# Optimization experiments

Measured on AMD Instinct MI355X. Metric: run time of the kernel, lower is better.

## Reference

```python
import jax, jax.numpy as jnp
import numpy as np

EPS = 1e-8

def setup_inputs() -> dict:
    key = jax.random.key(0)
    ks = jax.random.split(key, 7)
    B, S, H, NH, V = 4, 2048, 1024, 8, 2048
    sc = 1.0 / np.sqrt(H)
    return {
        "hidden": jax.random.normal(ks[0], (B, S, H), jnp.float32),
        "prior_w": jax.random.normal(ks[1], (H, NH), jnp.float32) * sc,
        "prior_b": jnp.zeros((NH,), jnp.float32),
        "latent_w": jax.random.normal(ks[2], (H, NH * H), jnp.float32) * sc,
        "latent_b": jnp.zeros((NH * H,), jnp.float32),
        "output_w": jax.random.normal(ks[3], (H, V), jnp.float32) * sc,
        "output_b": jnp.zeros((V,), jnp.float32),
    }

def reference(hidden, prior_w, prior_b, latent_w, latent_b, output_w, output_b):
    B, S, H = hidden.shape
    NH = prior_w.shape[1]
    # prior: sigmoid then renormalize over heads
    prior = jax.nn.sigmoid(hidden @ prior_w + prior_b)              # [B,S,NH]
    prior = prior / (prior.sum(-1, keepdims=True) + EPS)
    # latent: linear -> [B,S,NH,H] -> tanh
    latent = jnp.tanh((hidden @ latent_w + latent_b).reshape(B, S, NH, H))
    # per-head softmax over vocab, weighted sum over heads
    logits = jnp.einsum('bsnh,hv->bsnv', latent, output_w) + output_b
    probs = jax.nn.softmax(logits, axis=-1)                          # [B,S,NH,V]
    return jnp.einsum('bsn,bsnv->bsv', prior, probs)
```

## Files before the change

### kernel.cpp

```cpp
#include <hip/hip_runtime.h>
#include <hip/hip_bf16.h>
#include <stdint.h>

typedef _Float16 f16;
typedef _Float16 f16x8 __attribute__((ext_vector_type(8)));
typedef _Float16 f16x4 __attribute__((ext_vector_type(4)));
typedef float f32x4 __attribute__((ext_vector_type(4)));
typedef float f32x16 __attribute__((ext_vector_type(16)));

#define T_TOK 8192
#define H_DIM 1024
#define NHEAD 8
#define V_DIM 2048

__device__ __forceinline__ void gload16(const void* g, void* l) {
  __builtin_amdgcn_global_load_lds(
      (const __attribute__((address_space(1))) void*)(uintptr_t)g,
      (__attribute__((address_space(3))) void*)(unsigned)(uintptr_t)l,
      16, 0, 0);
}

__device__ __forceinline__ float fast_tanh(float x) {
  float xc = fminf(fmaxf(x, -12.f), 12.f);
  float e = __expf(2.f * xc);
  return (e - 1.f) / (e + 1.f);
}

__device__ __forceinline__ void stage_half(const f16* __restrict__ gRowBase,
                                           char* ldsHalf, int tid, int sl8,
                                           int Kd) {
  const int srow = tid >> 3;
  char* wuni = ldsHalf + ((tid >> 6) << 10);
  gload16(gRowBase + (size_t)srow * Kd + sl8, wuni);
  gload16(gRowBase + (size_t)(srow + 64) * Kd + sl8, wuni + 8192);
}

template <int TANH>
__global__ __launch_bounds__(512, 2) void k_gemm(const f16* __restrict__ A,
                                                 const f16* __restrict__ Bt,
                                                 const float* __restrict__ bias,
                                                 f16* __restrict__ C,
                                                 int M, int N, int K) {
  __shared__ __align__(16) f16 sA[2][16384];
  __shared__ __align__(16) f16 sB[2][16384];
  const int tid = threadIdx.x;
  const int lane = tid & 63;
  const int wid = tid >> 6;
  const int wr = wid >> 2, wc = wid & 3;
  const int id = blockIdx.y * 8 + blockIdx.x;
  const int cpx = gridDim.y;
  const int sw = (id & 7) * cpx + (id >> 3);
  const int m0 = (sw >> 3) * 256;
  const int n0 = blockIdx.z * 2048 + (sw & 7) * 256;
  const int NT = K >> 6;
  const int sl8 = ((tid & 7) ^ ((tid >> 3) & 7)) << 3;
  const int rr31 = lane & 31;
  const int hi = lane >> 5;
  const int l7 = lane & 7;

  const f16* Ag = A + (size_t)m0 * K;
  const f16* Bg = Bt + (size_t)n0 * K;
  char* sAb = (char*)&sA[0][0];
  char* sBb = (char*)&sB[0][0];

  stage_half(Ag, sAb, tid, sl8, K);
  stage_half(Ag + (size_t)128 * K, sAb + 16384, tid, sl8, K);
  stage_half(Bg, sBb, tid, sl8, K);
  stage_half(Bg + (size_t)128 * K, sBb + 16384, tid, sl8, K);
  stage_half(Bg + 64, sBb + 32768, tid, sl8, K);
  stage_half(Bg + (size_t)128 * K + 64, sBb + 32768 + 16384, tid, sl8, K);
  asm volatile("s_waitcnt vmcnt(4)" ::: "memory");
  __builtin_amdgcn_s_barrier();
  __builtin_amdgcn_sched_barrier(0);

  f32x16 acc[4][2] = {};
  f16x8 af0[4], af1[4], bf[2][4];

#define LDA_SET(dst, base, q)                                                  \
  {                                                                            \
    _Pragma("unroll") for (int mi = 0; mi < 4; ++mi) {                         \
      dst[mi] = *(const f16x8*)((base) + wr * 16384 + mi * 4096 + rr31 * 128 + \
                                (((2 * (q) + hi) ^ l7) << 4));                 \
    }                                                                          \
  }
#define LDB(base)                                                              \
  {                                                                            \
    _Pragma("unroll") for (int n = 0; n < 2; ++n) {                            \
      _Pragma("unroll") for (int ks = 0; ks < 4; ++ks) {                       \
        bf[n][ks] = *(const f16x8*)((base) + wc * 8192 + n * 4096 +            \
                                    rr31 * 128 + (((2 * ks + hi) ^ l7) << 4)); \
      }                                                                        \
    }                                                                          \
  }
#define MFMA8(ks, S)                                                           \
  {                                                                            \
    __builtin_amdgcn_s_setprio(1);                                             \
    _Pragma("unroll") for (int mi = 0; mi < 4; ++mi) {                         \
      _Pragma("unroll") for (int n = 0; n < 2; ++n) {                          \
        acc[mi][n] = __builtin_amdgcn_mfma_f32_32x32x16_f16(                   \
            S[mi], bf[n][ks], acc[mi][n], 0, 0, 0);                            \
      }                                                                        \
    }                                                                          \
    __builtin_amdgcn_s_setprio(0);                                             \
  }

  LDA_SET(af0, sAb, 0);

#define HALF(tt, bc)                                                           \
  {                                                                            \
    const char* cA = sAb + (bc)*32768;                                         \
    const char* cB = sBb + (bc)*32768;                                         \
    char* nA = sAb + ((bc) ^ 1) * 32768;                                       \
    char* nB = sBb + (bc)*32768;                                               \
    const int ktA = ((tt) + 1) << 6, ktB = ((tt) + 2) << 6;                    \
    const bool doA = (tt) + 1 < NT, doB = (tt) + 2 < NT;                       \
                                                                      \
    if (doA) stage_half(Ag + ktA, nA, tid, sl8, K);                            \
    LDB(cB);                                                                   \
    LDA_SET(af1, cA, 1);                                                       \
    __builtin_amdgcn_sched_barrier(0);                                         \
    MFMA8(0, af0);                                                             \
    __builtin_amdgcn_s_barrier();                                              \
                                                                      \
    if (doA) stage_half(Ag + (size_t)128 * K + ktA, nA + 16384, tid, sl8, K);  \
    LDA_SET(af0, cA, 2);                                                       \
    __builtin_amdgcn_sched_barrier(0);                                         \
    MFMA8(1, af1);                                                             \
    __builtin_amdgcn_s_barrier();                                              \
                                                                      \
    if (doB) stage_half(Bg + ktB, nB, tid, sl8, K);                            \
    LDA_SET(af1, cA, 3);                                                       \
    __builtin_amdgcn_sched_barrier(0);                                         \
    MFMA8(2, af0);                                                             \
    __builtin_amdgcn_s_barrier();                                              \
                  \
    if (doB) stage_half(Bg + (size_t)128 * K + ktB, nB + 16384, tid, sl8, K);  \
    if (doB) {                                                                 \
      asm volatile("s_waitcnt vmcnt(4)" ::: "memory");                         \
    } else {                                                                   \
      asm volatile("s_waitcnt vmcnt(0)" ::: "memory");                         \
    }                                                                          \
    __builtin_amdgcn_s_barrier();                                              \
    __builtin_amdgcn_sched_barrier(0);                                         \
    if (doA) LDA_SET(af0, sAb + ((bc) ^ 1) * 32768, 0);                        \
    __builtin_amdgcn_sched_barrier(0);                                         \
    MFMA8(3, af1);                                                             \
  }

#pragma unroll 1
  for (int T = 0; T < NT; T += 2) {
    HALF(T, 0);
    HALF(T + 1, 1);
  }
#undef HALF
#undef LDA_SET
#undef LDB
#undef MFMA8

  const int ccol0 = n0 + wc * 64 + rr31;
  float bv[2];
#pragma unroll
  for (int n = 0; n < 2; ++n) bv[n] = bias[ccol0 + n * 32];
#pragma unroll
  for (int mi = 0; mi < 4; ++mi) {
#pragma unroll
    for (int rq = 0; rq < 4; ++rq) {
#pragma unroll
      for (int r2 = 0; r2 < 4; ++r2) {
        const int row = m0 + wr * 128 + mi * 32 + r2 + 8 * rq + 4 * hi;
        f16* Crow = C + (size_t)row * N;
#pragma unroll
        for (int n = 0; n < 2; ++n) {
          float v = acc[mi][n][rq * 4 + r2] + bv[n];
          if (TANH) v = fast_tanh(v);
          Crow[ccol0 + n * 32] = (f16)v;
        }
      }
    }
  }
}

__global__ __launch_bounds__(256) void k_transpose(const float* __restrict__ in,
                                                   f16* __restrict__ out,
                                                   int R, int C) {
  __shared__ f16 tile[64][66];
  const int c0 = blockIdx.x * 64, r0 = blockIdx.y * 64;
  const int tid = threadIdx.x;
  const int tr = tid >> 4;
  const int tc4 = (tid & 15) * 4;
#pragma unroll
  for (int i = 0; i < 4; ++i) {
    const int r = tr + i * 16;
    const float4 v = *(const float4*)&in[(size_t)(r0 + r) * C + c0 + tc4];
    tile[tc4 + 0][r] = (f16)v.x;
    tile[tc4 + 1][r] = (f16)v.y;
    tile[tc4 + 2][r] = (f16)v.z;
    tile[tc4 + 3][r] = (f16)v.w;
  }
  __syncthreads();
  const int oc = tid >> 2;
  const int or4 = (tid & 3) * 16;
#pragma unroll
  for (int i = 0; i < 4; ++i) {
    f16x4 w;
    w[0] = tile[oc][or4 + i * 4 + 0];
    w[1] = tile[oc][or4 + i * 4 + 1];
    w[2] = tile[oc][or4 + i * 4 + 2];
    w[3] = tile[oc][or4 + i * 4 + 3];
    *(f16x4*)&out[(size_t)(c0 + oc) * R + r0 + or4 + i * 4] = w;
  }
}

__global__ __launch_bounds__(256) void k_prior_conv(const float* __restrict__ hidden,
                                                    const float* __restrict__ pw,
                                                    const float* __restrict__ pb,
                                                    float* __restrict__ prior,
                                                    f16* __restrict__ hidden_h) {
  const int wid = threadIdx.x >> 6, lane = threadIdx.x & 63;
  const int t = blockIdx.x * 4 + wid;
  const float* hrow = hidden + (size_t)t * H_DIM;
  f16* orow = hidden_h + (size_t)t * H_DIM;
  float acc[NHEAD] = {0.f, 0.f, 0.f, 0.f, 0.f, 0.f, 0.f, 0.f};
#pragma unroll
  for (int i = 0; i < 4; ++i) {
    const int k = i * 256 + lane * 4;
    const float4 v = *(const float4*)(hrow + k);
    f16x4 o;
    o[0] = (f16)v.x; o[1] = (f16)v.y; o[2] = (f16)v.z; o[3] = (f16)v.w;
    *(f16x4*)(orow + k) = o;
    const float vv[4] = {v.x, v.y, v.z, v.w};
#pragma unroll
    for (int j = 0; j < 4; ++j) {
      const float* wr = pw + (size_t)(k + j) * NHEAD;
#pragma unroll
      for (int h = 0; h < NHEAD; ++h) acc[h] += vv[j] * wr[h];
    }
  }
#pragma unroll
  for (int h = 0; h < NHEAD; ++h) {
#pragma unroll
    for (int off = 32; off >= 1; off >>= 1) acc[h] += __shfl_xor(acc[h], off);
  }
  if (lane == 0) {
    float p[NHEAD], s = 0.f;
#pragma unroll
    for (int h = 0; h < NHEAD; ++h) {
      p[h] = 1.f / (1.f + __expf(-(acc[h] + pb[h])));
      s += p[h];
    }
    float inv = 1.f / (s + 1e-8f);
#pragma unroll
    for (int h = 0; h < NHEAD; ++h) prior[t * NHEAD + h] = p[h] * inv;
  }
}

__global__ __launch_bounds__(256) void k_softmax(const f16* __restrict__ logits,
                                                 const float* __restrict__ prior,
                                                 float* __restrict__ out,
                                                 int t0) {
  __shared__ float redsm[NHEAD * 4];
  const int tl = blockIdx.x;
  const int t = t0 + tl;
  const int tid = threadIdx.x, lane = tid & 63, wid = tid >> 6;
  const f16* base = logits + (size_t)tl * NHEAD * V_DIM + tid * 8;

  f16x8 x[NHEAD];
#pragma unroll
  for (int h = 0; h < NHEAD; ++h) x[h] = *(const f16x8*)(base + h * V_DIM);

  float xv[NHEAD][8];
  float sml[NHEAD];
#pragma unroll
  for (int h = 0; h < NHEAD; ++h) {
    float s = 0.f;
#pragma unroll
    for (int j = 0; j < 8; ++j) {
      xv[h][j] = __expf(fminf((float)x[h][j], 50.f));
      s += xv[h][j];
    }
    sml[h] = s;
  }
#pragma unroll
  for (int h = 0; h < NHEAD; ++h) {
#pragma unroll
    for (int off = 32; off >= 1; off >>= 1) sml[h] += __shfl_xor(sml[h], off);
  }
  if (lane == 0) {
#pragma unroll
    for (int h = 0; h < NHEAD; ++h) redsm[h * 4 + wid] = sml[h];
  }
  __syncthreads();

  float oa[8] = {0.f, 0.f, 0.f, 0.f, 0.f, 0.f, 0.f, 0.f};
#pragma unroll
  for (int h = 0; h < NHEAD; ++h) {
    const float s = redsm[h * 4 + 0] + redsm[h * 4 + 1] + redsm[h * 4 + 2] +
                    redsm[h * 4 + 3];
    const float coef = prior[t * NHEAD + h] / s;
#pragma unroll
    for (int j = 0; j < 8; ++j) oa[j] += coef * xv[h][j];
  }
  float4* op = (float4*)(out + (size_t)t * V_DIM + tid * 8);
  op[0] = make_float4(oa[0], oa[1], oa[2], oa[3]);
  op[1] = make_float4(oa[4], oa[5], oa[6], oa[7]);
}

extern "C" void kernel_launch(void* const* d_in, const int* in_sizes, int n_in,
                              void* d_out, int out_size, void* d_ws, size_t ws_size,
                              hipStream_t stream) {
  const float* hidden   = (const float*)d_in[0];
  const float* prior_w  = (const float*)d_in[1];
  const float* prior_b  = (const float*)d_in[2];
  const float* latent_w = (const float*)d_in[3];
  const float* latent_b = (const float*)d_in[4];
  const float* output_w = (const float*)d_in[5];
  const float* output_b = (const float*)d_in[6];
  float* out = (float*)d_out;

  char* ws = (char*)d_ws;
  size_t off = 0;
  auto alloc = [&](size_t bytes) -> void* {
    void* p = ws + off;
    off += (bytes + 255) & ~(size_t)255;
    return p;
  };
  f16* hidden_h = (f16*)alloc((size_t)T_TOK * H_DIM * 2);
  f16* lw_t     = (f16*)alloc((size_t)NHEAD * H_DIM * H_DIM * 2);
  f16* ow_t     = (f16*)alloc((size_t)V_DIM * H_DIM * 2);
  float* prior  = (float*)alloc((size_t)T_TOK * NHEAD * 4);
  f16* latent_h = (f16*)alloc((size_t)T_TOK * NHEAD * H_DIM * 2);

  int TQ = 2048;
  while (TQ > 256 && off + (size_t)TQ * NHEAD * V_DIM * 2 > ws_size) TQ >>= 1;
  f16* logits_q = (f16*)alloc((size_t)TQ * NHEAD * V_DIM * 2);

  k_prior_conv<<<T_TOK / 4, 256, 0, stream>>>(hidden, prior_w, prior_b, prior,
                                              hidden_h);
  k_transpose<<<dim3(NHEAD * H_DIM / 64, H_DIM / 64), 256, 0, stream>>>(
      latent_w, lw_t, H_DIM, NHEAD * H_DIM);
  k_transpose<<<dim3(V_DIM / 64, H_DIM / 64), 256, 0, stream>>>(
      output_w, ow_t, H_DIM, V_DIM);

  k_gemm<1><<<dim3(8, T_TOK / 256, 4), 512, 0, stream>>>(
      hidden_h, lw_t, latent_b, latent_h, T_TOK, NHEAD * H_DIM, H_DIM);

  const int nq = T_TOK / TQ;
  for (int s = 0; s < nq; ++s) {
    const int MR = TQ * NHEAD;
    k_gemm<0><<<dim3(8, MR / 256, 1), 512, 0, stream>>>(
        latent_h + (size_t)s * MR * H_DIM, ow_t, output_b, logits_q, MR, V_DIM,
        H_DIM);
    k_softmax<<<TQ, 256, 0, stream>>>(logits_q, prior, out, s * TQ);
  }
}
```

Baseline: 597.9 us.

## Switch GEMM to 16x16x32 MFMA and chunk latent/logits pipeline by token

The GEMM's inner product now uses 16x16x32 f16 MFMA instructions with an 8x4 grid of 4-wide accumulators instead of 32x32x16 with 4x2 16-wide accumulators. The LDS fragment addressing and the epilogue row/column mapping are rewritten to match. The host side also processes tokens in chunks: the latent GEMM, logits GEMM and softmax run per chunk. This shrinks the latent and logits buffers so they are more likely to stay cache resident, and avoids materialising the whole latent tensor. The cost is more kernel launches and possibly different MFMA throughput and register pressure.

```diff
diff --git a/kernel.cpp b/kernel.cpp
--- a/kernel.cpp
+++ b/kernel.cpp
@@ -6,7 +6,6 @@
 typedef _Float16 f16x8 __attribute__((ext_vector_type(8)));
 typedef _Float16 f16x4 __attribute__((ext_vector_type(4)));
 typedef float f32x4 __attribute__((ext_vector_type(4)));
-typedef float f32x16 __attribute__((ext_vector_type(16)));
 
 #define T_TOK 8192
 #define H_DIM 1024
@@ -54,9 +53,9 @@
   const int n0 = blockIdx.z * 2048 + (sw & 7) * 256;
   const int NT = K >> 6;
   const int sl8 = ((tid & 7) ^ ((tid >> 3) & 7)) << 3;
-  const int rr31 = lane & 31;
-  const int hi = lane >> 5;
-  const int l7 = lane & 7;
+  const int lo15 = lane & 15;
+  const int offk0 = lo15 * 128 + (((lane >> 4)) ^ (lane & 7)) * 16;
+  const int offk1 = lo15 * 128 + ((4 + (lane >> 4)) ^ (lane & 7)) * 16;
 
   const f16* Ag = A + (size_t)m0 * K;
   const f16* Bg = Bt + (size_t)n0 * K;
@@ -73,33 +72,35 @@
   __builtin_amdgcn_s_barrier();
   __builtin_amdgcn_sched_barrier(0);
 
-  f32x16 acc[4][2] = {};
-  f16x8 af0[4], af1[4], bf[2][4];
+  f32x4 acc[8][4] = {};
+  f16x8 af0[4], af1[4], bf[4][2];
 
 #define LDA_SET(dst, base, q)                                                  \
   {                                                                            \
-    _Pragma("unroll") for (int mi = 0; mi < 4; ++mi) {                         \
-      dst[mi] = *(const f16x8*)((base) + wr * 16384 + mi * 4096 + rr31 * 128 + \
-                                (((2 * (q) + hi) ^ l7) << 4));                 \
-    }                                                                          \
+    dst[0] = *(const f16x8*)((base) + wr * 16384 + (2 * (q) + 0) * 2048 + offk0); \
+    dst[1] = *(const f16x8*)((base) + wr * 16384 + (2 * (q) + 0) * 2048 + offk1); \
+    dst[2] = *(const f16x8*)((base) + wr * 16384 + (2 * (q) + 1) * 2048 + offk0); \
+    dst[3] = *(const f16x8*)((base) + wr * 16384 + (2 * (q) + 1) * 2048 + offk1); \
   }
 #define LDB(base)                                                              \
   {                                                                            \
-    _Pragma("unroll") for (int n = 0; n < 2; ++n) {                            \
-      _Pragma("unroll") for (int ks = 0; ks < 4; ++ks) {                       \
-        bf[n][ks] = *(const f16x8*)((base) + wc * 8192 + n * 4096 +            \
-                                    rr31 * 128 + (((2 * ks + hi) ^ l7) << 4)); \
-      }                                                                        \
+    _Pragma("unroll") for (int ni = 0; ni < 4; ++ni) {                         \
+      bf[ni][0] = *(const f16x8*)((base) + wc * 8192 + ni * 2048 + offk0);     \
+      bf[ni][1] = *(const f16x8*)((base) + wc * 8192 + ni * 2048 + offk1);     \
     }                                                                          \
   }
-#define MFMA8(ks, S)                                                           \
+#define MFMA16(q, S)                                                           \
   {                                                                            \
     __builtin_amdgcn_s_setprio(1);                                             \
-    _Pragma("unroll") for (int mi = 0; mi < 4; ++mi) {                         \
-      _Pragma("unroll") for (int n = 0; n < 2; ++n) {                          \
-        acc[mi][n] = __builtin_amdgcn_mfma_f32_32x32x16_f16(                   \
-            S[mi], bf[n][ks], acc[mi][n], 0, 0, 0);                            \
-      }                                                                        \
+    _Pragma("unroll") for (int ni = 0; ni < 4; ++ni) {                         \
+      acc[2 * (q) + 0][ni] = __builtin_amdgcn_mfma_f32_16x16x32_f16(           \
+          S[0], bf[ni][0], acc[2 * (q) + 0][ni], 0, 0, 0);                     \
+      acc[2 * (q) + 0][ni] = __builtin_amdgcn_mfma_f32_16x16x32_f16(           \
+          S[1], bf[ni][1], acc[2 * (q) + 0][ni], 0, 0, 0);                     \
+      acc[2 * (q) + 1][ni] = __builtin_amdgcn_mfma_f32_16x16x32_f16(           \
+          S[2], bf[ni][0], acc[2 * (q) + 1][ni], 0, 0, 0);                     \
+      acc[2 * (q) + 1][ni] = __builtin_amdgcn_mfma_f32_16x16x32_f16(           \
+          S[3], bf[ni][1], acc[2 * (q) + 1][ni], 0, 0, 0);                     \
     }                                                                          \
     __builtin_amdgcn_s_setprio(0);                                             \
   }
@@ -114,24 +115,24 @@
     char* nB = sBb + (bc)*32768;                                               \
     const int ktA = ((tt) + 1) << 6, ktB = ((tt) + 2) << 6;                    \
     const bool doA = (tt) + 1 < NT, doB = (tt) + 2 < NT;                       \
-                                                                      \
+                                    \
     if (doA) stage_half(Ag + ktA, nA, tid, sl8, K);                            \
     LDB(cB);                                                                   \
     LDA_SET(af1, cA, 1);                                                       \
     __builtin_amdgcn_sched_barrier(0);                                         \
-    MFMA8(0, af0);                                                             \
+    MFMA16(0, af0);                                                            \
     __builtin_amdgcn_s_barrier();                                              \
                                                                       \
     if (doA) stage_half(Ag + (size_t)128 * K + ktA, nA + 16384, tid, sl8, K);  \
     LDA_SET(af0, cA, 2);                                                       \
     __builtin_amdgcn_sched_barrier(0);                                         \
-    MFMA8(1, af1);                                                             \
+    MFMA16(1, af1);                                                            \
     __builtin_amdgcn_s_barrier();                                              \
                                                                       \
     if (doB) stage_half(Bg + ktB, nB, tid, sl8, K);                            \
     LDA_SET(af1, cA, 3);                                                       \
     __builtin_amdgcn_sched_barrier(0);                                         \
-    MFMA8(2, af0);                                                             \
+    MFMA16(2, af0);                                                            \
     __builtin_amdgcn_s_barrier();                                              \
                   \
     if (doB) stage_half(Bg + (size_t)128 * K + ktB, nB + 16384, tid, sl8, K);  \
@@ -144,7 +145,7 @@
     __builtin_amdgcn_sched_barrier(0);                                         \
     if (doA) LDA_SET(af0, sAb + ((bc) ^ 1) * 32768, 0);                        \
     __builtin_amdgcn_sched_barrier(0);                                         \
-    MFMA8(3, af1);                                                             \
+    MFMA16(3, af1);                                                            \
   }
 
 #pragma unroll 1
@@ -155,26 +156,23 @@
 #undef HALF
 #undef LDA_SET
 #undef LDB
-#undef MFMA8
-
-  const int ccol0 = n0 + wc * 64 + rr31;
-  float bv[2];
-#pragma unroll
-  for (int n = 0; n < 2; ++n) bv[n] = bias[ccol0 + n * 32];
-#pragma unroll
-  for (int mi = 0; mi < 4; ++mi) {
-#pragma unroll
-    for (int rq = 0; rq < 4; ++rq) {
-#pragma unroll
-      for (int r2 = 0; r2 < 4; ++r2) {
-        const int row = m0 + wr * 128 + mi * 32 + r2 + 8 * rq + 4 * hi;
-        f16* Crow = C + (size_t)row * N;
-#pragma unroll
-        for (int n = 0; n < 2; ++n) {
-          float v = acc[mi][n][rq * 4 + r2] + bv[n];
-          if (TANH) v = fast_tanh(v);
-          Crow[ccol0 + n * 32] = (f16)v;
-        }
+#undef MFMA16
+
+  const int crow = m0 + wr * 128 + ((lane >> 4) << 2);
+  const int ccol0 = n0 + wc * 64 + lo15;
+  float bv[4];
+#pragma unroll
+  for (int ni = 0; ni < 4; ++ni) bv[ni] = bias[ccol0 + ni * 16];
+#pragma unroll
+  for (int mi = 0; mi < 8; ++mi) {
+#pragma unroll
+    for (int r = 0; r < 4; ++r) {
+      f16* Crow = C + (size_t)(crow + mi * 16 + r) * N;
+#pragma unroll
+      for (int ni = 0; ni < 4; ++ni) {
+        float v = acc[mi][ni][r] + bv[ni];
+        if (TANH) v = fast_tanh(v);
+        Crow[ccol0 + ni * 16] = (f16)v;
       }
     }
   }
@@ -328,11 +326,15 @@
   f16* lw_t     = (f16*)alloc((size_t)NHEAD * H_DIM * H_DIM * 2);
   f16* ow_t     = (f16*)alloc((size_t)V_DIM * H_DIM * 2);
   float* prior  = (float*)alloc((size_t)T_TOK * NHEAD * 4);
-  f16* latent_h = (f16*)alloc((size_t)T_TOK * NHEAD * H_DIM * 2);
-
-  int TQ = 2048;
-  while (TQ > 256 && off + (size_t)TQ * NHEAD * V_DIM * 2 > ws_size) TQ >>= 1;
-  f16* logits_q = (f16*)alloc((size_t)TQ * NHEAD * V_DIM * 2);
+
+  int TC = T_TOK / 2;
+  while (TC > 256 &&
+         off + (size_t)TC * NHEAD * H_DIM * 2 + 256 +
+                 (size_t)TC * NHEAD * V_DIM * 2 >
+             ws_size)
+    TC >>= 1;
+  f16* latent_c = (f16*)alloc((size_t)TC * NHEAD * H_DIM * 2);
+  f16* logits_c = (f16*)alloc((size_t)TC * NHEAD * V_DIM * 2);
 
   k_prior_conv<<<T_TOK / 4, 256, 0, stream>>>(hidden, prior_w, prior_b, prior,
                                               hidden_h);
@@ -341,15 +343,13 @@
   k_transpose<<<dim3(V_DIM / 64, H_DIM / 64), 256, 0, stream>>>(
       output_w, ow_t, H_DIM, V_DIM);
 
-  k_gemm<1><<<dim3(8, T_TOK / 256, 4), 512, 0, stream>>>(
-      hidden_h, lw_t, latent_b, latent_h, T_TOK, NHEAD * H_DIM, H_DIM);
-
-  const int nq = T_TOK / TQ;
-  for (int s = 0; s < nq; ++s) {
-    const int MR = TQ * NHEAD;
-    k_gemm<0><<<dim3(8, MR / 256, 1), 512, 0, stream>>>(
-        latent_h + (size_t)s * MR * H_DIM, ow_t, output_b, logits_q, MR, V_DIM,
-        H_DIM);
-    k_softmax<<<TQ, 256, 0, stream>>>(logits_q, prior, out, s * TQ);
-  }
-}
+  const int nchunk = T_TOK / TC;
+  for (int s = 0; s < nchunk; ++s) {
+    k_gemm<1><<<dim3(8, TC / 256, 4), 512, 0, stream>>>(
+        hidden_h + (size_t)s * TC * H_DIM, lw_t, latent_b, latent_c, TC,
+        NHEAD * H_DIM, H_DIM);
+    k_gemm<0><<<dim3(8, TC * NHEAD / 256, 1), 512, 0, stream>>>(
+        latent_c, ow_t, output_b, logits_c, TC * NHEAD, V_DIM, H_DIM);
+    k_softmax<<<TC, 256, 0, stream>>>(logits_c, prior, out, s * TC);
+  }
+}
```

Measured after the change: 542.7 us. 9.2% less time.
